# Kernel optimization log

Measured on AMD Instinct MI355X. Metric: run time of the kernel, lower is better.

## Reference

```python
import jax, jax.numpy as jnp
import numpy as np

N_NODES = 50000
N_EDGES = 600000
F_NODE = 128
F_EDGE = 32
MSG = 32


def setup_inputs() -> dict:
    key = jax.random.key(0)
    k1, k2, k3, k4, k5, k6, k7 = jax.random.split(key, 7)
    node_features = jax.random.normal(k1, (N_NODES, F_NODE), dtype=jnp.float32)
    edge_node_indices = jax.random.randint(k2, (2, N_EDGES), 0, N_NODES, dtype=jnp.int64)
    edge_features = jax.random.normal(k3, (N_EDGES, F_EDGE), dtype=jnp.float32)
    edge_in = 2 * F_NODE + F_EDGE  # 288
    node_in = F_NODE + MSG  # 160
    s_e = 1.0 / np.sqrt(edge_in)
    s_n = 1.0 / np.sqrt(node_in)
    We = jax.random.uniform(k4, (edge_in, MSG), dtype=jnp.float32, minval=-s_e, maxval=s_e)
    be = jax.random.uniform(k5, (MSG,), dtype=jnp.float32, minval=-s_e, maxval=s_e)
    Wn = jax.random.uniform(k6, (node_in, F_NODE), dtype=jnp.float32, minval=-s_n, maxval=s_n)
    bn = jax.random.uniform(k7, (F_NODE,), dtype=jnp.float32, minval=-s_n, maxval=s_n)
    return {
        "node_features": node_features,
        "edge_node_indices": edge_node_indices,
        "edge_features": edge_features,
        "We": We, "be": be, "Wn": Wn, "bn": bn,
    }


def reference(node_features, edge_node_indices, edge_features, We, be, Wn, bn):
    node0, node1 = edge_node_indices[0], edge_node_indices[1]
    # gather endpoint features per edge: [E, 2*Fn + Fe]
    msg_in = jnp.concatenate(
        [node_features[node0], node_features[node1], edge_features], axis=1
    )
    messages = jax.nn.relu(msg_in @ We + be)  # [E, MSG]
    # scatter-sum messages into source nodes (scatter index = node0)
    msg_sums = jax.ops.segment_sum(messages, node0, num_segments=node_features.shape[0])
    node_in = jnp.concatenate([node_features, msg_sums], axis=1)  # [N, Fn+MSG]
    return jax.nn.relu(node_in @ Wn + bn)  # [N, Fn]
```

## Files before the change

kernel.cpp:

```cpp
#include <hip/hip_runtime.h>

#define N_NODES 50000
#define N_EDGES 600000
#define F_NODE 128
#define F_EDGE 32
#define MSG 32
#define NPB 32
#define CHK 128
#define QB64 ((N_NODES + 63) / 64)
#define FBLOCKS ((N_NODES + NPB - 1) / NPB)
#define CBLOCKS ((N_EDGES + 255) / 256)

typedef float v2f __attribute__((ext_vector_type(2)));

__device__ __forceinline__ unsigned short f2bf(float f) {
    union { float f; unsigned int u; } v; v.f = f;
    unsigned int r = v.u + 0x7fffu + ((v.u >> 16) & 1u);
    return (unsigned short)(r >> 16);
}

#define BAR_LGKM() do {                                           \
    asm volatile("s_waitcnt lgkmcnt(0)" ::: "memory");            \
    __builtin_amdgcn_s_barrier();                                 \
    asm volatile("" ::: "memory");                                \
} while (0)

__global__ __launch_bounds__(256)
void hist_kernel(const float* __restrict__ nf,
                 const float* __restrict__ We,
                 const float* __restrict__ be,
                 const int* __restrict__ idx,
                 unsigned short* __restrict__ Q,
                 unsigned short* __restrict__ P0g,
                 int* __restrict__ deg,
                 int* __restrict__ rank)
{
    if (blockIdx.x >= QB64) {
        int e = (blockIdx.x - QB64) * 256 + threadIdx.x;
        if (e < N_EDGES) {
            int n = idx[e];
            if ((unsigned)n >= (unsigned)N_NODES) n = 0;
            rank[e] = atomicAdd(&deg[n], 1);
        }
        return;
    }
    __shared__ float sInT[32 * 64];
    __shared__ float sWeA[32 * 32];
    __shared__ float sWeB[32 * 32];

    const int tid = threadIdx.x;
    const int n0b = blockIdx.x * 64;
    const int ng = tid & 31;
    const int og = tid >> 5;

    v2f accA[4], accB[4];
#pragma unroll
    for (int j = 0; j < 4; ++j) { accA[j] = (v2f){0.f, 0.f}; accB[j] = (v2f){0.f, 0.f}; }

    for (int kc = 0; kc < 4; ++kc) {
        __syncthreads();
        ((float4*)sWeA)[tid] = ((const float4*)(We + kc * 32 * MSG))[tid];
        ((float4*)sWeB)[tid] = ((const float4*)(We + (128 + kc * 32) * MSG))[tid];
        {
            int nl = tid >> 2, q = tid & 3;
            int n = n0b + nl; if (n >= N_NODES) n = N_NODES - 1;
            const float4* src4 = (const float4*)(nf + (size_t)n * F_NODE + kc * 32);
#pragma unroll
            for (int h = 0; h < 2; ++h) {
                float4 v = src4[q * 2 + h];
                int kl = q * 8 + h * 4;
                sInT[(kl + 0) * 64 + nl] = v.x;
                sInT[(kl + 1) * 64 + nl] = v.y;
                sInT[(kl + 2) * 64 + nl] = v.z;
                sInT[(kl + 3) * 64 + nl] = v.w;
            }
        }
        __syncthreads();
#pragma unroll
        for (int k = 0; k < 32; ++k) {
            v2f m = *(const v2f*)&sInT[k * 64 + 2 * ng];
            float4 wa = *(const float4*)&sWeA[k * 32 + og * 4];
            float4 wb = *(const float4*)&sWeB[k * 32 + og * 4];
            accA[0] += m * wa.x; accA[1] += m * wa.y;
            accA[2] += m * wa.z; accA[3] += m * wa.w;
            accB[0] += m * wb.x; accB[1] += m * wb.y;
            accB[2] += m * wb.z; accB[3] += m * wb.w;
        }
    }
    float bloc[4];
#pragma unroll
    for (int j = 0; j < 4; ++j) bloc[j] = be[og * 4 + j];
#pragma unroll
    for (int i = 0; i < 2; ++i) {
        int n = n0b + 2 * ng + i;
        if (n < N_NODES) {
            ushort4 oq, op;
            oq.x = f2bf(accB[0][i]); oq.y = f2bf(accB[1][i]);
            oq.z = f2bf(accB[2][i]); oq.w = f2bf(accB[3][i]);
            op.x = f2bf(accA[0][i] + bloc[0]); op.y = f2bf(accA[1][i] + bloc[1]);
            op.z = f2bf(accA[2][i] + bloc[2]); op.w = f2bf(accA[3][i] + bloc[3]);
            *(ushort4*)(Q   + (size_t)n * MSG + og * 4) = oq;
            *(ushort4*)(P0g + (size_t)n * MSG + og * 4) = op;
        }
    }
}

__global__ __launch_bounds__(1024)
void scan_kernel(int* __restrict__ deg_cursor) {
    __shared__ int wsum[16];
    __shared__ int wpre[16];
    const int t = threadIdx.x;
    const int lane = t & 63;
    const int wid = t >> 6;
    const int N4 = N_NODES / 4;
    const int NT = (N4 + 1023) / 1024;
    int run = 0;
    int4 vnext = make_int4(0, 0, 0, 0);
    if (t < N4) vnext = ((const int4*)deg_cursor)[t];
    for (int tt = 0; tt < NT; ++tt) {
        int4 v = vnext;
        if (tt + 1 < NT) {
            int ni = (tt + 1) * 1024 + t;
            vnext = (ni < N4) ? ((const int4*)deg_cursor)[ni] : make_int4(0, 0, 0, 0);
        }
        int s = v.x + v.y + v.z + v.w;
        int x = s;
#pragma unroll
        for (int d = 1; d < 64; d <<= 1) {
            int u = __shfl_up(x, (unsigned)d, 64);
            if (lane >= d) x += u;
        }
        if (lane == 63) wsum[wid] = x;
        BAR_LGKM();
        if (wid == 0) {
            int ss = (lane < 16) ? wsum[lane] : 0;
#pragma unroll
            for (int d = 1; d < 16; d <<= 1) {
                int u = __shfl_up(ss, (unsigned)d, 64);
                if (lane >= d) ss += u;
            }
            if (lane < 16) wpre[lane] = ss;
        }
        BAR_LGKM();
        int wexcl = (wid > 0) ? wpre[wid - 1] : 0;
        int total = wpre[15];
        int i4 = tt * 1024 + t;
        if (i4 < N4) {
            int base = run + wexcl + (x - s);
            int4 o;
            o.x = base;
            o.y = base + v.x;
            o.z = base + v.x + v.y;
            o.w = base + v.x + v.y + v.z;
            ((int4*)deg_cursor)[i4] = o;
        }
        run += total;
        BAR_LGKM();
    }
}

__global__ void place_kernel(const int* __restrict__ idx,
                             const int* __restrict__ startArr,
                             const int* __restrict__ rank,
                             int* __restrict__ perm) {
    int e = blockIdx.x * 256 + threadIdx.x;
    if (e < N_EDGES) {
        int n = idx[e];
        if ((unsigned)n >= (unsigned)N_NODES) n = 0;
        int p = startArr[n] + rank[e];
        if ((unsigned)p < (unsigned)N_EDGES) perm[p] = e;
    }
}

__global__ __launch_bounds__(256, 4)
void fused_kernel(const float* __restrict__ nf,
                  const int* __restrict__ idx,
                  const float* __restrict__ ef,
                  const float* __restrict__ We,
                  const float* __restrict__ Wn,
                  const float* __restrict__ bn,
                  const int* __restrict__ perm,
                  const int* __restrict__ startArr,
                  const unsigned short* __restrict__ Q,
                  const unsigned short* __restrict__ P0g,
                  float* __restrict__ out)
{
    __shared__ __align__(16) float S[5796];
    float* sBuf = S;
    float* sWeC = S + 4096;
    float* sInT2 = S + 4096;
    unsigned short* sP0h = (unsigned short*)(S + 5120);
    int* sOff = (int*)(S + 5632);
    int* sNL  = (int*)(S + 5665);

    const int tid = threadIdx.x;
    const int n0b = blockIdx.x * NPB;

    if (tid <= NPB) {
        int nn = n0b + tid;
        int v = (nn < N_NODES) ? startArr[nn] : N_EDGES;
        if (v < 0) v = 0;
        if (v > N_EDGES) v = N_EDGES;
        sOff[tid] = v;
    }
    ((float4*)sWeC)[tid] = ((const float4*)(We + 256 * MSG))[tid];
    if (tid < 128) {
        int r = tid >> 2, c = (tid & 3) * 8;
        int n = n0b + r; if (n >= N_NODES) n = N_NODES - 1;
        *(uint4*)(sP0h + r * MSG + c) = *(const uint4*)(P0g + (size_t)n * MSG + c);
    }
    __syncthreads();

    const int rs = sOff[0];
    const int re = sOff[NPB];

    float msum[4];
#pragma unroll
    for (int j = 0; j < 4; ++j) msum[j] = 0.f;
    const int rnl = tid >> 3;
    const int rq4 = (tid & 7) * 4;
    const int gx  = (rq4 >> 3) << 2;

    const int eg = tid & 63;
    const int og = tid >> 6;
    const int el = tid >> 1;
    const int h2 = tid & 1;

    int n1r = 0;
    int pe_next = 0, pe_next2 = 0;
    float4 efr[4];
#pragma unroll
    for (int q = 0; q < 4; ++q) efr[q] = make_float4(0.f, 0.f, 0.f, 0.f);

    if (rs < re) {
        int e0 = rs + el;
        int pe0 = 0;
        if (e0 < re) {
            pe0 = perm[e0];
            if ((unsigned)pe0 >= (unsigned)N_EDGES) pe0 = 0;
            if (h2 == 0) {
                int tn = idx[N_EDGES + pe0];
                if ((unsigned)tn >= (unsigned)N_NODES) tn = 0;
                n1r = tn;
            }
        }
        const float4* ef4 = (const float4*)(ef + (size_t)pe0 * F_EDGE + h2 * 16);
#pragma unroll
        for (int q = 0; q < 4; ++q) efr[q] = ef4[q];
        int e1 = rs + CHK + el;
        if (e1 < re) {
            int p = perm[e1];
            if ((unsigned)p >= (unsigned)N_EDGES) p = 0;
            pe_next = p;
        }
        pe_next2 = pe_next;
    }

    for (int cs = rs; cs < re; cs += CHK) {
        BAR_LGKM();
        pe_next = pe_next2;
        {
#pragma unroll
            for (int q = 0; q < 4; ++q) {
                float4 v = efr[q];
                int g = (h2 * 2 + (q >> 1)) & 3;
                int ctw = ((el & ~3) ^ (g << 2)) + (el & 3);
                int r0 = (h2 * 16 + q * 4) * CHK;
                sBuf[r0 + 0 * CHK + ctw] = v.x;
                sBuf[r0 + 1 * CHK + ctw] = v.y;
                sBuf[r0 + 2 * CHK + ctw] = v.z;
                sBuf[r0 + 3 * CHK + ctw] = v.w;
            }
            if (h2 == 0) {
                int e = cs + el;
                int ln = 0;
                if (e < re) {
                    int lo = 0, hi = NPB;
#pragma unroll
                    for (int s = 0; s < 5; ++s) {
                        int mid = (lo + hi) >> 1;
                        if (sOff[mid] <= e) lo = mid; else hi = mid;
                    }
                    ln = lo;
                }
                sNL[el] = (ln << 20) | n1r;
            }
            int e1 = cs + CHK + el;
            if (e1 < re) {
                int pe1 = pe_next;
                if (h2 == 0) {
                    int tn = idx[N_EDGES + pe1];
                    if ((unsigned)tn >= (unsigned)N_NODES) tn = 0;
                    n1r = tn;
                }
                const float4* ef4 = (const float4*)(ef + (size_t)pe1 * F_EDGE + h2 * 16);
#pragma unroll
                for (int q = 0; q < 4; ++q) efr[q] = ef4[q];
            } else if (h2 == 0) n1r = 0;
            int e2 = cs + 2 * CHK + el;
            if (e2 < re) {
                int p = perm[e2];
                if ((unsigned)p >= (unsigned)N_EDGES) p = 0;
                pe_next2 = p;
            } else pe_next2 = 0;
        }
        BAR_LGKM();

        int nlv0 = sNL[2 * eg], nlv1 = sNL[2 * eg + 1];
        uint4 qv[2];
        qv[0] = *(const uint4*)(Q + (size_t)(nlv0 & 0xFFFFF) * MSG + og * 8);
        qv[1] = *(const uint4*)(Q + (size_t)(nlv1 & 0xFFFFF) * MSG + og * 8);

        v2f accv[8];
#pragma unroll
        for (int j = 0; j < 8; ++j) accv[j] = (v2f){0.f, 0.f};

        const float* weB = sWeC + og * 8;
#pragma unroll
        for (int k = 0; k < 32; ++k) {
            int mb = k * CHK + (((2 * eg) & ~3) ^ (((k >> 3) & 3) << 2)) + ((2 * eg) & 3);
            v2f m = *(const v2f*)&sBuf[mb];
            float4 w0 = *(const float4*)&weB[k * 32];
            float4 w1 = *(const float4*)&weB[k * 32 + 4];
            accv[0] += m * w0.x; accv[1] += m * w0.y;
            accv[2] += m * w0.z; accv[3] += m * w0.w;
            accv[4] += m * w1.x; accv[5] += m * w1.y;
            accv[6] += m * w1.z; accv[7] += m * w1.w;
        }

        BAR_LGKM();

        {
            uint4 pv[2];
            pv[0] = *(const uint4*)(sP0h + (nlv0 >> 20) * MSG + og * 8);
            pv[1] = *(const uint4*)(sP0h + (nlv1 >> 20) * MSG + og * 8);
            int sb = (((2 * eg) & ~3) ^ (og << 2)) + ((2 * eg) & 3);
#pragma unroll
            for (int j = 0; j < 8; ++j) {
                float sv[2];
#pragma unroll
                for (int i = 0; i < 2; ++i) {
                    unsigned qu = ((const unsigned*)&qv[i])[j >> 1];
                    unsigned pu = ((const unsigned*)&pv[i])[j >> 1];
                    float qf = __uint_as_float((j & 1) ? (qu & 0xffff0000u) : (qu << 16));
                    float pf = __uint_as_float((j & 1) ? (pu & 0xffff0000u) : (pu << 16));
                    sv[i] = fmaxf(accv[j][i] + pf + qf, 0.f);
                }
                float2 s2; s2.x = sv[0]; s2.y = sv[1];
                *(float2*)&sBuf[(og * 8 + j) * CHK + sb] = s2;
            }
        }
        BAR_LGKM();

        {
            int lo = sOff[rnl] - cs;     if (lo < 0) lo = 0;
            int hi = sOff[rnl + 1] - cs; if (hi > CHK) hi = CHK;
            for (int elr = lo; elr < hi; ++elr) {
                int ebase = ((elr & ~3) ^ gx) + (elr & 3);
#pragma unroll
                for (int j = 0; j < 4; ++j)
                    msum[j] += sBuf[(rq4 + j) * CHK + ebase];
            }
        }
    }

    const int ng2 = tid & 31;
    const int og2 = tid >> 5;

    v2f acc2v[8];
#pragma unroll
    for (int j = 0; j < 8; ++j) acc2v[j] = (v2f){0.f, 0.f};

    for (int kc = 0; kc < 5; ++kc) {
        __syncthreads();
        {
            const float4* w4 = (const float4*)(Wn + (size_t)kc * 32 * 128);
            float4* s4 = (float4*)sBuf;
#pragma unroll
            for (int i = 0; i < 4; ++i) s4[tid + 256 * i] = w4[tid + 256 * i];
        }
        {
            if (kc < 4) {
                int nl = tid >> 3, q = tid & 7;
                int n = n0b + nl; if (n >= N_NODES) n = N_NODES - 1;
                float4 v = *(const float4*)(nf + (size_t)n * F_NODE + kc * 32 + q * 4);
#pragma unroll
                for (int h = 0; h < 4; ++h) {
                    int r = q * 4 + h;
                    sInT2[r * 32 + (nl ^ ((r & 7) << 2))] = (&v.x)[h];
                }
            } else {
#pragma unroll
                for (int h = 0; h < 4; ++h) {
                    int r = rq4 + h;
                    sInT2[r * 32 + (rnl ^ ((r & 7) << 2))] = msum[h];
                }
            }
        }
        __syncthreads();

#pragma unroll
        for (int k = 0; k < 32; ++k) {
            float m = sInT2[k * 32 + (ng2 ^ ((k & 7) << 2))];
            const float* wr = &sBuf[k * 128 + og2 * 16];
            float4 w0 = *(const float4*)&wr[0];
            float4 w1 = *(const float4*)&wr[4];
            float4 w2 = *(const float4*)&wr[8];
            float4 w3 = *(const float4*)&wr[12];
            v2f wp[8] = { {w0.x,w0.y},{w0.z,w0.w},{w1.x,w1.y},{w1.z,w1.w},
                          {w2.x,w2.y},{w2.z,w2.w},{w3.x,w3.y},{w3.z,w3.w} };
#pragma unroll
            for (int h = 0; h < 8; ++h) acc2v[h] += wp[h] * m;
        }
    }

    {
        int n = n0b + ng2;
        if (n < N_NODES) {
            float* dst = out + (size_t)n * F_NODE + og2 * 16;
#pragma unroll
            for (int j = 0; j < 16; j += 4) {
                float4 v;
                v.x = fmaxf(acc2v[(j + 0) >> 1][0] + bn[og2 * 16 + j + 0], 0.f);
                v.y = fmaxf(acc2v[(j + 1) >> 1][1] + bn[og2 * 16 + j + 1], 0.f);
                v.z = fmaxf(acc2v[(j + 2) >> 1][0] + bn[og2 * 16 + j + 2], 0.f);
                v.w = fmaxf(acc2v[(j + 3) >> 1][1] + bn[og2 * 16 + j + 3], 0.f);
                *(float4*)(dst + j) = v;
            }
        }
    }
}

extern "C" void kernel_launch(void* const* d_in, const int* in_sizes, int n_in,
                              void* d_out, int out_size, void* d_ws, size_t ws_size,
                              hipStream_t stream) {
    const float* nf  = (const float*)d_in[0];
    const int*   idx = (const int*)d_in[1];
    const float* ef  = (const float*)d_in[2];
    const float* We  = (const float*)d_in[3];
    const float* be  = (const float*)d_in[4];
    const float* Wn  = (const float*)d_in[5];
    const float* bn  = (const float*)d_in[6];
    float* out = (float*)d_out;

    int* deg  = (int*)d_ws;
    int* rank = deg + N_NODES;
    int* perm = rank + N_EDGES;
    unsigned short* Q   = (unsigned short*)(perm + N_EDGES);
    unsigned short* P0g = Q + (size_t)N_NODES * MSG;

    hipMemsetAsync(deg, 0, (size_t)N_NODES * sizeof(int), stream);

    hist_kernel<<<QB64 + CBLOCKS, 256, 0, stream>>>(nf, We, be, idx, Q, P0g, deg, rank);
    scan_kernel<<<1, 1024, 0, stream>>>(deg);
    place_kernel<<<CBLOCKS, 256, 0, stream>>>(idx, deg, rank, perm);

    fused_kernel<<<FBLOCKS, 256, 0, stream>>>(
        nf, idx, ef, We, Wn, bn, perm, deg, Q, P0g, out);
}
```

Before: 271.9 us.

## Double-buffer message tile and use 4x4 register tiles in edge and node GEMMs

Moves computed messages into a separate shared buffer (sMsg) so the edge-feature tile and message tile no longer alias, removing two barriers per chunk. Edge-GEMM and node-GEMM thread mappings change from 2x8 and 1x16 per-thread tiles to 4x4 tiles with float4 LDS reads for both operands, cutting shared-memory load instructions per FMA. Shared memory grows from about 23KB to about 40KB per block, which could reduce occupancy, and the new output store pattern writes 16-byte pieces per node row.

```diff
diff --git a/kernel.cpp b/kernel.cpp
--- a/kernel.cpp
+++ b/kernel.cpp
@@ -185,13 +185,15 @@
                   const unsigned short* __restrict__ P0g,
                   float* __restrict__ out)
 {
-    __shared__ __align__(16) float S[5796];
+    __shared__ __align__(16) float S[9892];
     float* sBuf = S;
-    float* sWeC = S + 4096;
+    float* sMsg = S + 4096;
+    float* sWeC = S + 8192;
+    unsigned short* sP0h = (unsigned short*)(S + 9216);
+    int* sNL  = (int*)(S + 9728);
+    int* sOff = (int*)(S + 9856);
+    float* sWn   = S;
     float* sInT2 = S + 4096;
-    unsigned short* sP0h = (unsigned short*)(S + 5120);
-    int* sOff = (int*)(S + 5632);
-    int* sNL  = (int*)(S + 5665);
 
     const int tid = threadIdx.x;
     const int n0b = blockIdx.x * NPB;
@@ -221,8 +223,9 @@
     const int rq4 = (tid & 7) * 4;
     const int gx  = (rq4 >> 3) << 2;
 
-    const int eg = tid & 63;
-    const int og = tid >> 6;
+    const int eq = tid & 31;
+    const int cq = tid >> 5;
+    const int g1 = (cq >> 1) & 3;
     const int el = tid >> 1;
     const int h2 = tid & 1;
 
@@ -257,7 +260,6 @@
     }
 
     for (int cs = rs; cs < re; cs += CHK) {
-        BAR_LGKM();
         pe_next = pe_next2;
         {
 #pragma unroll
@@ -306,48 +308,47 @@
         }
         BAR_LGKM();
 
-        int nlv0 = sNL[2 * eg], nlv1 = sNL[2 * eg + 1];
-        uint4 qv[2];
-        qv[0] = *(const uint4*)(Q + (size_t)(nlv0 & 0xFFFFF) * MSG + og * 8);
-        qv[1] = *(const uint4*)(Q + (size_t)(nlv1 & 0xFFFFF) * MSG + og * 8);
-
-        v2f accv[8];
-#pragma unroll
-        for (int j = 0; j < 8; ++j) accv[j] = (v2f){0.f, 0.f};
-
-        const float* weB = sWeC + og * 8;
+        int4 nlq = *(const int4*)&sNL[4 * eq];
+        int nlv[4] = { nlq.x, nlq.y, nlq.z, nlq.w };
+        uint2 qv[4];
+#pragma unroll
+        for (int i = 0; i < 4; ++i)
+            qv[i] = *(const uint2*)(Q + (size_t)(nlv[i] & 0xFFFFF) * MSG + cq * 4);
+
+        v2f accp[4][2];
+#pragma unroll
+        for (int j = 0; j < 4; ++j) { accp[j][0] = (v2f){0.f,0.f}; accp[j][1] = (v2f){0.f,0.f}; }
+
 #pragma unroll
         for (int k = 0; k < 32; ++k) {
-            int mb = k * CHK + (((2 * eg) & ~3) ^ (((k >> 3) & 3) << 2)) + ((2 * eg) & 3);
-            v2f m = *(const v2f*)&sBuf[mb];
-            float4 w0 = *(const float4*)&weB[k * 32];
-            float4 w1 = *(const float4*)&weB[k * 32 + 4];
-            accv[0] += m * w0.x; accv[1] += m * w0.y;
-            accv[2] += m * w0.z; accv[3] += m * w0.w;
-            accv[4] += m * w1.x; accv[5] += m * w1.y;
-            accv[6] += m * w1.z; accv[7] += m * w1.w;
-        }
-
-        BAR_LGKM();
-
-        {
-            uint4 pv[2];
-            pv[0] = *(const uint4*)(sP0h + (nlv0 >> 20) * MSG + og * 8);
-            pv[1] = *(const uint4*)(sP0h + (nlv1 >> 20) * MSG + og * 8);
-            int sb = (((2 * eg) & ~3) ^ (og << 2)) + ((2 * eg) & 3);
-#pragma unroll
-            for (int j = 0; j < 8; ++j) {
-                float sv[2];
-#pragma unroll
-                for (int i = 0; i < 2; ++i) {
-                    unsigned qu = ((const unsigned*)&qv[i])[j >> 1];
-                    unsigned pu = ((const unsigned*)&pv[i])[j >> 1];
+            float4 m4 = *(const float4*)&sBuf[k * CHK + ((4 * eq) ^ (((k >> 3) & 3) << 2))];
+            float4 w  = *(const float4*)&sWeC[k * 32 + cq * 4];
+            v2f m01 = (v2f){m4.x, m4.y}, m23 = (v2f){m4.z, m4.w};
+            accp[0][0] += m01 * w.x; accp[0][1] += m23 * w.x;
+            accp[1][0] += m01 * w.y; accp[1][1] += m23 * w.y;
+            accp[2][0] += m01 * w.z; accp[2][1] += m23 * w.z;
+            accp[3][0] += m01 * w.w; accp[3][1] += m23 * w.w;
+        }
+
+        {
+            uint2 pv[4];
+#pragma unroll
+            for (int i = 0; i < 4; ++i)
+                pv[i] = *(const uint2*)(sP0h + (nlv[i] >> 20) * MSG + cq * 4);
+            int sb = (4 * eq) ^ (g1 << 2);
+#pragma unroll
+            for (int j = 0; j < 4; ++j) {
+                float sv[4];
+#pragma unroll
+                for (int i = 0; i < 4; ++i) {
+                    unsigned qu = (j < 2) ? qv[i].x : qv[i].y;
+                    unsigned pu = (j < 2) ? pv[i].x : pv[i].y;
                     float qf = __uint_as_float((j & 1) ? (qu & 0xffff0000u) : (qu << 16));
                     float pf = __uint_as_float((j & 1) ? (pu & 0xffff0000u) : (pu << 16));
-                    sv[i] = fmaxf(accv[j][i] + pf + qf, 0.f);
-                }
-                float2 s2; s2.x = sv[0]; s2.y = sv[1];
-                *(float2*)&sBuf[(og * 8 + j) * CHK + sb] = s2;
+                    sv[i] = fmaxf(accp[j][i >> 1][i & 1] + pf + qf, 0.f);
+                }
+                *(float4*)&sMsg[(cq * 4 + j) * CHK + sb] =
+                    make_float4(sv[0], sv[1], sv[2], sv[3]);
             }
         }
         BAR_LGKM();
@@ -359,23 +360,23 @@
                 int ebase = ((elr & ~3) ^ gx) + (elr & 3);
 #pragma unroll
                 for (int j = 0; j < 4; ++j)
-                    msum[j] += sBuf[(rq4 + j) * CHK + ebase];
-            }
-        }
-    }
-
-    const int ng2 = tid & 31;
-    const int og2 = tid >> 5;
-
-    v2f acc2v[8];
-#pragma unroll
-    for (int j = 0; j < 8; ++j) acc2v[j] = (v2f){0.f, 0.f};
+                    msum[j] += sMsg[(rq4 + j) * CHK + ebase];
+            }
+        }
+    }
+
+    const int png = tid & 7;
+    const int pcg = tid >> 3;
+
+    v2f acc2[4][2];
+#pragma unroll
+    for (int j = 0; j < 4; ++j) { acc2[j][0] = (v2f){0.f,0.f}; acc2[j][1] = (v2f){0.f,0.f}; }
 
     for (int kc = 0; kc < 5; ++kc) {
         __syncthreads();
         {
             const float4* w4 = (const float4*)(Wn + (size_t)kc * 32 * 128);
-            float4* s4 = (float4*)sBuf;
+            float4* s4 = (float4*)sWn;
 #pragma unroll
             for (int i = 0; i < 4; ++i) s4[tid + 256 * i] = w4[tid + 256 * i];
         }
@@ -401,33 +402,32 @@
 
 #pragma unroll
         for (int k = 0; k < 32; ++k) {
-            float m = sInT2[k * 32 + (ng2 ^ ((k & 7) << 2))];
-            const float* wr = &sBuf[k * 128 + og2 * 16];
-            float4 w0 = *(const float4*)&wr[0];
-            float4 w1 = *(const float4*)&wr[4];
-            float4 w2 = *(const float4*)&wr[8];
-            float4 w3 = *(const float4*)&wr[12];
-            v2f wp[8] = { {w0.x,w0.y},{w0.z,w0.w},{w1.x,w1.y},{w1.z,w1.w},
-                          {w2.x,w2.y},{w2.z,w2.w},{w3.x,w3.y},{w3.z,w3.w} };
-#pragma unroll
-            for (int h = 0; h < 8; ++h) acc2v[h] += wp[h] * m;
+            float4 m4 = *(const float4*)&sInT2[k * 32 + ((4 * png) ^ ((k & 7) << 2))];
+            float4 w  = *(const float4*)&sWn[k * 128 + 4 * pcg];
+            v2f m01 = (v2f){m4.x, m4.y}, m23 = (v2f){m4.z, m4.w};
+            acc2[0][0] += m01 * w.x; acc2[0][1] += m23 * w.x;
+            acc2[1][0] += m01 * w.y; acc2[1][1] += m23 * w.y;
+            acc2[2][0] += m01 * w.z; acc2[2][1] += m23 * w.z;
+            acc2[3][0] += m01 * w.w; acc2[3][1] += m23 * w.w;
         }
     }
 
     {
-        int n = n0b + ng2;
-        if (n < N_NODES) {
-            float* dst = out + (size_t)n * F_NODE + og2 * 16;
-#pragma unroll
-            for (int j = 0; j < 16; j += 4) {
-                float4 v;
-                v.x = fmaxf(acc2v[(j + 0) >> 1][0] + bn[og2 * 16 + j + 0], 0.f);
-                v.y = fmaxf(acc2v[(j + 1) >> 1][1] + bn[og2 * 16 + j + 1], 0.f);
-                v.z = fmaxf(acc2v[(j + 2) >> 1][0] + bn[og2 * 16 + j + 2], 0.f);
-                v.w = fmaxf(acc2v[(j + 3) >> 1][1] + bn[og2 * 16 + j + 3], 0.f);
-                *(float4*)(dst + j) = v;
-            }
-        }
+        float4 bnv = *(const float4*)(bn + 4 * pcg);
+#pragma unroll
+        for (int p = 0; p < 2; ++p)
+#pragma unroll
+            for (int l = 0; l < 2; ++l) {
+                int n = n0b + 4 * png + 2 * p + l;
+                if (n < N_NODES) {
+                    float4 v;
+                    v.x = fmaxf(acc2[0][p][l] + bnv.x, 0.f);
+                    v.y = fmaxf(acc2[1][p][l] + bnv.y, 0.f);
+                    v.z = fmaxf(acc2[2][p][l] + bnv.z, 0.f);
+                    v.w = fmaxf(acc2[3][p][l] + bnv.w, 0.f);
+                    *(float4*)(out + (size_t)n * F_NODE + 4 * pcg) = v;
+                }
+            }
     }
 }
 
```

After: 260.3 us. 4.3% less time.
